# Performance work log

Measured on AMD Instinct MI355X. Metric: run time of the kernel, lower is better.

The kernel has to match this reference:

```python
import jax, jax.numpy as jnp
import numpy as np

# dims: B=batch, S=seq len, H=heads, D=in_features per head, R=realizations, K=conv kernel
B, S, H, D, R, K = 2, 1024, 8, 64, 32, 128


def setup_inputs() -> dict:
    key = jax.random.key(0)
    kq, kk, kwq, kwk, kz = jax.random.split(key, 5)
    queries = jax.random.normal(kq, (B, S, H, D), jnp.float32)
    keys = jax.random.normal(kk, (B, S, H, D), jnp.float32)
    # depthwise conv weights, torch init: uniform[0,1), shape (C_out, 1, K) with groups=C_out
    wq = jax.random.uniform(kwq, (H * D, 1, K), jnp.float32)
    wk = jax.random.uniform(kwk, (H * D, 1, K), jnp.float32)
    # stochastic process noise z: (B*R, H*D, 4K+S), scaled by 1/sqrt(R*D)
    z = jax.random.normal(kz, (B * R, H * D, 4 * K + S), jnp.float32) / np.float32(np.sqrt(R * D))
    return {"queries": queries, "keys": keys, "wq": wq, "wk": wk, "z": z}


def _dwconv(x, w):
    # depthwise 1D cross-correlation, VALID padding (matches nn.Conv1d, groups=C)
    return jax.lax.conv_general_dilated(
        x, w, window_strides=(1,), padding='VALID',
        dimension_numbers=('NCH', 'OIH', 'NCH'),
        feature_group_count=w.shape[0])


def reference(queries, keys, wq, wk, z):
    # note the faithful swap from the source: kbar uses conv_q, qbar uses conv_k
    kbar = _dwconv(z, wq)[:, :, K:K + S].reshape(B, R, H, D, S)
    qbar = _dwconv(z, wk)[:, :, K:K + S].reshape(B, R, H, D, S)
    # fused broadcast-multiply + feature-dim reduction:
    # (qbar * queries[:,None]).sum(axis=3) then permute -> (B,S,H,R)
    qhat = jnp.einsum('brhds,bshd->bshr', qbar, queries)
    khat = jnp.einsum('brhds,bshd->bshr', kbar, keys)
    return qhat, khat
```

## Files before the change

kernel.cpp:

```cpp
#include <hip/hip_runtime.h>

#define BB 2
#define SS 1024
#define HH 8
#define DD 64
#define RR 32
#define KK 128
#define ZLEN 1536
#define HD 512

#define MS 256
#define DC 16
#define NTC 24
#define WROWS 192
#define WSEG (WROWS*DC)
#define PARTS_FLOATS (256*8*2*64*16)

typedef _Float16 f16x8 __attribute__((ext_vector_type(8)));
typedef _Float16 f16x2 __attribute__((ext_vector_type(2)));
typedef float    f32x16 __attribute__((ext_vector_type(16)));

__device__ __forceinline__ void dma16h(const _Float16* g, _Float16* l) {
    const int lane = threadIdx.x & 63;
    __builtin_amdgcn_global_load_lds(
        (const __attribute__((address_space(1))) void*)(g + lane * 8),
        (__attribute__((address_space(3))) void*)l, 16, 0, 0);
}

__global__ __launch_bounds__(256) void wprep_kernel(
    const float* __restrict__ wq, const float* __restrict__ wk,
    _Float16* __restrict__ wqG, _Float16* __restrict__ wkG)
{
    const int tid = threadIdx.x;
    const int h = blockIdx.x & 7, dc = blockIdx.x >> 3;
    #pragma unroll
    for (int i = 0; i < 12; ++i) {
        const int idx = i * 256 + tid;
        const int ti = idx >> 4, di = idx & 15;
        const int tau = ti - 32;
        float vq = 0.f, vk = 0.f;
        if (tau >= 0 && tau < KK) {
            const int src = (h * 64 + dc * 16 + di) * KK + tau;
            vq = wq[src]; vk = wk[src];
        }
        const int dst = (h * 4 + dc) * WSEG + idx;
        wqG[dst] = (_Float16)vq; wkG[dst] = (_Float16)vk;
    }
}

__global__ __launch_bounds__(512) void convspe_mfma(
    const float* __restrict__ q, const float* __restrict__ kmat,
    const _Float16* __restrict__ wqG, const _Float16* __restrict__ wkG,
    const float* __restrict__ z, float* __restrict__ parts)
{
    __shared__ __align__(16) _Float16 zbuf[2][16 * 32 * 16];
    __shared__ __align__(16) _Float16 wqs[WSEG];
    __shared__ __align__(16) _Float16 wks[WSEG];

    const int tid  = threadIdx.x;
    const int wave = tid >> 6;
    const int lane = tid & 63;
    const int rl   = lane & 31;
    const int hi   = lane >> 5;

    const int bx = blockIdx.x;
    const int dc = bx & 3, stile = (bx >> 2) & 3, h = (bx >> 4) & 7, b = bx >> 7;
    const int s0b = stile * MS;
    const int d0  = dc * DC;

    if (wave == 0) {
        const _Float16* seg = wqG + (h * 4 + dc) * WSEG;
        #pragma unroll
        for (int i = 0; i < 6; ++i) dma16h(seg + i * 512, wqs + i * 512);
    } else if (wave == 1) {
        const _Float16* seg = wkG + (h * 4 + dc) * WSEG;
        #pragma unroll
        for (int i = 0; i < 6; ++i) dma16h(seg + i * 512, wks + i * 512);
    }

    f16x8 qf, kf;
    {
        const int s = s0b + wave * 32 + rl;
        const size_t base = (((size_t)b * SS + s) * HH + h) * DD + d0 + 8 * hi;
        #pragma unroll
        for (int j = 0; j < 8; ++j) {
            qf[j] = (_Float16)q[base + j];
            kf[j] = (_Float16)kmat[base + j];
        }
    }

    const int sr  = tid >> 4;
    const int sth = (tid >> 3) & 1;
    const int sdp = tid & 7;
    const float* zr0 = z + ((size_t)(b * RR + sr) * HD + h * DD + d0 + 2 * sdp) * ZLEN
                         + KK + s0b + sth * 8;
    const float* zr1 = zr0 + ZLEN;

    float4 ra[2], rb[2];
    auto loadchunk = [&](int tc) {
        const float4* p0 = (const float4*)(zr0 + tc * 16);
        const float4* p1 = (const float4*)(zr1 + tc * 16);
        #pragma unroll
        for (int i = 0; i < 2; ++i) { ra[i] = p0[i]; rb[i] = p1[i]; }
    };
    auto writechunk = [&](int p) {
        f16x2* dst = (f16x2*)zbuf[p];
        #pragma unroll
        for (int i = 0; i < 2; ++i) {
            const float av[4] = {ra[i].x, ra[i].y, ra[i].z, ra[i].w};
            const float bv[4] = {rb[i].x, rb[i].y, rb[i].z, rb[i].w};
            #pragma unroll
            for (int e = 0; e < 4; ++e) {
                const int ts = sth * 8 + i * 4 + e;
                dst[(ts * 32 + sr) * 8 + sdp] =
                    __builtin_bit_cast(f16x2, __builtin_amdgcn_cvt_pkrtz(av[e], bv[e]));
            }
        }
    };

    f32x16 accq, acck;
    #pragma unroll
    for (int j = 0; j < 16; ++j) { accq[j] = 0.f; acck[j] = 0.f; }

    loadchunk(0);
    writechunk(0);
    loadchunk(1);
    __syncthreads();

    for (int tc = 0; tc < NTC; ++tc) {
        const int p = tc & 1;
        const int tqbase = tc * 16 - wave * 32;
        #pragma unroll 1
        for (int ts = 0; ts < 16; ++ts) {
            const int tau_s = tqbase + ts;
            if (tau_s < 0 || tau_s >= 160) continue;
            const f16x8 a = *(const f16x8*)&zbuf[p][(ts * 32 + rl) * 16 + 8 * hi];
            const int row = tau_s - rl + 32;
            const f16x8 wkf = *(const f16x8*)&wks[row * 16 + 8 * hi];
            const f16x8 wqf = *(const f16x8*)&wqs[row * 16 + 8 * hi];
            accq = __builtin_amdgcn_mfma_f32_32x32x16_f16(a, wkf * qf, accq, 0, 0, 0);
            acck = __builtin_amdgcn_mfma_f32_32x32x16_f16(a, wqf * kf, acck, 0, 0, 0);
        }
        if (tc + 1 < NTC) writechunk((tc + 1) & 1);
        if (tc + 2 < NTC) loadchunk(tc + 2);
        __syncthreads();
    }

    {
        float* pq = parts + ((((size_t)bx * 8 + wave) * 2 + 0) * 64 + lane) * 16;
        float* pk = parts + ((((size_t)bx * 8 + wave) * 2 + 1) * 64 + lane) * 16;
        #pragma unroll
        for (int g = 0; g < 4; ++g) {
            *(float4*)&pq[g * 4] = make_float4(accq[4*g], accq[4*g+1], accq[4*g+2], accq[4*g+3]);
            *(float4*)&pk[g * 4] = make_float4(acck[4*g], acck[4*g+1], acck[4*g+2], acck[4*g+3]);
        }
    }
}

__global__ __launch_bounds__(256) void reduce_kernel(
    const float* __restrict__ parts, float* __restrict__ out)
{
    const int idx = blockIdx.x * 256 + threadIdx.x;
    const int rq = idx & 7, h = (idx >> 3) & 7, s = (idx >> 6) & 1023;
    const int b = (idx >> 16) & 1, o = idx >> 17;
    const int stile = s >> 8, sub = (s >> 5) & 7, rl = s & 31;

    float acc4[4] = {0.f, 0.f, 0.f, 0.f};
    #pragma unroll
    for (int dc = 0; dc < 4; ++dc) {
        const int bx = ((b * 8 + h) * 4 + stile) * 4 + dc;
        const float* pb = parts + (((size_t)bx * 8 + sub) * 2 + o) * 1024;
        #pragma unroll
        for (int i = 0; i < 4; ++i) {
            const int r = rq * 4 + i;
            const int hi2 = (r >> 2) & 1;
            const int reg = (r & 3) + 4 * (r >> 3);
            acc4[i] += pb[(hi2 * 32 + rl) * 16 + reg];
        }
    }
    *(float4*)&out[(size_t)idx * 4] = make_float4(acc4[0], acc4[1], acc4[2], acc4[3]);
}

extern "C" void kernel_launch(void* const* d_in, const int* in_sizes, int n_in,
                              void* d_out, int out_size, void* d_ws, size_t ws_size,
                              hipStream_t stream) {
    const float* q  = (const float*)d_in[0];
    const float* k  = (const float*)d_in[1];
    const float* wq = (const float*)d_in[2];
    const float* wk = (const float*)d_in[3];
    const float* z  = (const float*)d_in[4];
    float* out = (float*)d_out;

    float* parts   = (float*)d_ws;
    _Float16* wqG  = (_Float16*)((char*)d_ws + (size_t)PARTS_FLOATS * 4);
    _Float16* wkG  = wqG + 8 * 4 * WSEG;

    hipLaunchKernelGGL(wprep_kernel, dim3(32), dim3(256), 0, stream, wq, wk, wqG, wkG);
    hipLaunchKernelGGL(convspe_mfma, dim3(256), dim3(512), 0, stream,
                       q, k, wqG, wkG, z, parts);
    hipLaunchKernelGGL(reduce_kernel, dim3(1024), dim3(256), 0, stream, parts, out);
}
```

Measured before the change: 322.6 us.

## Fuse weight prep into conv kernel, software-pipeline MFMA loop, vectorize reduce

Removes the separate weight-prep kernel and has each conv block convert and stage its own fp16 weight slice, with zero padding, directly into LDS. The first z chunk load is issued before the q/k loads so those latencies overlap. The inner MFMA loop drops the per-iteration bounds test by computing the valid range up front and double-buffers its LDS reads in registers. The reduce kernel now reads each partial with one float4 instead of four scalar loads. The cost is redundant weight conversion across the blocks that share a head and d-chunk, plus higher register pressure from the prefetched operands.

```diff
diff --git a/kernel.cpp b/kernel.cpp
--- a/kernel.cpp
+++ b/kernel.cpp
@@ -20,37 +20,9 @@
 typedef _Float16 f16x2 __attribute__((ext_vector_type(2)));
 typedef float    f32x16 __attribute__((ext_vector_type(16)));
 
-__device__ __forceinline__ void dma16h(const _Float16* g, _Float16* l) {
-    const int lane = threadIdx.x & 63;
-    __builtin_amdgcn_global_load_lds(
-        (const __attribute__((address_space(1))) void*)(g + lane * 8),
-        (__attribute__((address_space(3))) void*)l, 16, 0, 0);
-}
-
-__global__ __launch_bounds__(256) void wprep_kernel(
-    const float* __restrict__ wq, const float* __restrict__ wk,
-    _Float16* __restrict__ wqG, _Float16* __restrict__ wkG)
-{
-    const int tid = threadIdx.x;
-    const int h = blockIdx.x & 7, dc = blockIdx.x >> 3;
-    #pragma unroll
-    for (int i = 0; i < 12; ++i) {
-        const int idx = i * 256 + tid;
-        const int ti = idx >> 4, di = idx & 15;
-        const int tau = ti - 32;
-        float vq = 0.f, vk = 0.f;
-        if (tau >= 0 && tau < KK) {
-            const int src = (h * 64 + dc * 16 + di) * KK + tau;
-            vq = wq[src]; vk = wk[src];
-        }
-        const int dst = (h * 4 + dc) * WSEG + idx;
-        wqG[dst] = (_Float16)vq; wkG[dst] = (_Float16)vk;
-    }
-}
-
 __global__ __launch_bounds__(512) void convspe_mfma(
     const float* __restrict__ q, const float* __restrict__ kmat,
-    const _Float16* __restrict__ wqG, const _Float16* __restrict__ wkG,
+    const float* __restrict__ wq, const float* __restrict__ wk,
     const float* __restrict__ z, float* __restrict__ parts)
 {
     __shared__ __align__(16) _Float16 zbuf[2][16 * 32 * 16];
@@ -58,7 +30,7 @@
     __shared__ __align__(16) _Float16 wks[WSEG];
 
     const int tid  = threadIdx.x;
-    const int wave = tid >> 6;
+    const int wave = __builtin_amdgcn_readfirstlane(tid >> 6);
     const int lane = tid & 63;
     const int rl   = lane & 31;
     const int hi   = lane >> 5;
@@ -67,27 +39,6 @@
     const int dc = bx & 3, stile = (bx >> 2) & 3, h = (bx >> 4) & 7, b = bx >> 7;
     const int s0b = stile * MS;
     const int d0  = dc * DC;
-
-    if (wave == 0) {
-        const _Float16* seg = wqG + (h * 4 + dc) * WSEG;
-        #pragma unroll
-        for (int i = 0; i < 6; ++i) dma16h(seg + i * 512, wqs + i * 512);
-    } else if (wave == 1) {
-        const _Float16* seg = wkG + (h * 4 + dc) * WSEG;
-        #pragma unroll
-        for (int i = 0; i < 6; ++i) dma16h(seg + i * 512, wks + i * 512);
-    }
-
-    f16x8 qf, kf;
-    {
-        const int s = s0b + wave * 32 + rl;
-        const size_t base = (((size_t)b * SS + s) * HH + h) * DD + d0 + 8 * hi;
-        #pragma unroll
-        for (int j = 0; j < 8; ++j) {
-            qf[j] = (_Float16)q[base + j];
-            kf[j] = (_Float16)kmat[base + j];
-        }
-    }
 
     const int sr  = tid >> 4;
     const int sth = (tid >> 3) & 1;
@@ -118,11 +69,40 @@
         }
     };
 
+    loadchunk(0);
+
+    f16x8 qf, kf;
+    {
+        const int s = s0b + wave * 32 + rl;
+        const size_t base = (((size_t)b * SS + s) * HH + h) * DD + d0 + 8 * hi;
+        #pragma unroll
+        for (int j = 0; j < 8; ++j) {
+            qf[j] = (_Float16)q[base + j];
+            kf[j] = (_Float16)kmat[base + j];
+        }
+    }
+
+    {
+        const int di = tid & 15, tq = tid >> 4;
+        const int grow = (h * DD + dc * DC + di) * KK + tq * 4;
+        const float4 vq4 = *(const float4*)&wq[grow];
+        const float4 vk4 = *(const float4*)&wk[grow];
+        const float aq[4] = {vq4.x, vq4.y, vq4.z, vq4.w};
+        const float ak[4] = {vk4.x, vk4.y, vk4.z, vk4.w};
+        #pragma unroll
+        for (int e = 0; e < 4; ++e) {
+            const int ds = (tq * 4 + e + 32) * 16 + di;
+            wqs[ds] = (_Float16)aq[e];
+            wks[ds] = (_Float16)ak[e];
+        }
+        wqs[tid] = (_Float16)0.f;        wks[tid] = (_Float16)0.f;
+        wqs[2560 + tid] = (_Float16)0.f; wks[2560 + tid] = (_Float16)0.f;
+    }
+
     f32x16 accq, acck;
     #pragma unroll
     for (int j = 0; j < 16; ++j) { accq[j] = 0.f; acck[j] = 0.f; }
 
-    loadchunk(0);
     writechunk(0);
     loadchunk(1);
     __syncthreads();
@@ -130,16 +110,33 @@
     for (int tc = 0; tc < NTC; ++tc) {
         const int p = tc & 1;
         const int tqbase = tc * 16 - wave * 32;
-        #pragma unroll 1
-        for (int ts = 0; ts < 16; ++ts) {
-            const int tau_s = tqbase + ts;
-            if (tau_s < 0 || tau_s >= 160) continue;
-            const f16x8 a = *(const f16x8*)&zbuf[p][(ts * 32 + rl) * 16 + 8 * hi];
-            const int row = tau_s - rl + 32;
-            const f16x8 wkf = *(const f16x8*)&wks[row * 16 + 8 * hi];
-            const f16x8 wqf = *(const f16x8*)&wqs[row * 16 + 8 * hi];
-            accq = __builtin_amdgcn_mfma_f32_32x32x16_f16(a, wkf * qf, accq, 0, 0, 0);
-            acck = __builtin_amdgcn_mfma_f32_32x32x16_f16(a, wqf * kf, acck, 0, 0, 0);
+        const int lo  = (tqbase < 0) ? -tqbase : 0;
+        const int hi_ = (160 - tqbase < 16) ? (160 - tqbase) : 16;
+        if (lo < hi_) {
+            const _Float16* zb = zbuf[p];
+            auto zrd = [&](int ts) {
+                return *(const f16x8*)&zb[(ts * 32 + rl) * 16 + 8 * hi];
+            };
+            auto wrd = [&](const _Float16* ws, int ts) {
+                const int row = tqbase + ts - rl + 32;
+                return *(const f16x8*)&ws[row * 16 + 8 * hi];
+            };
+            f16x8 a0 = zrd(lo), k0 = wrd(wks, lo), q0 = wrd(wqs, lo);
+            f16x8 a1 = a0, k1 = k0, q1 = q0;
+            if (lo + 1 < hi_) { a1 = zrd(lo + 1); k1 = wrd(wks, lo + 1); q1 = wrd(wqs, lo + 1); }
+            for (int ts = lo; ts < hi_ - 2; ++ts) {
+                const f16x8 a2 = zrd(ts + 2), k2 = wrd(wks, ts + 2), q2 = wrd(wqs, ts + 2);
+                accq = __builtin_amdgcn_mfma_f32_32x32x16_f16(a0, k0 * qf, accq, 0, 0, 0);
+                acck = __builtin_amdgcn_mfma_f32_32x32x16_f16(a0, q0 * kf, acck, 0, 0, 0);
+                a0 = a1; k0 = k1; q0 = q1;
+                a1 = a2; k1 = k2; q1 = q2;
+            }
+            accq = __builtin_amdgcn_mfma_f32_32x32x16_f16(a0, k0 * qf, accq, 0, 0, 0);
+            acck = __builtin_amdgcn_mfma_f32_32x32x16_f16(a0, q0 * kf, acck, 0, 0, 0);
+            if (lo + 1 < hi_) {
+                accq = __builtin_amdgcn_mfma_f32_32x32x16_f16(a1, k1 * qf, accq, 0, 0, 0);
+                acck = __builtin_amdgcn_mfma_f32_32x32x16_f16(a1, q1 * kf, acck, 0, 0, 0);
+            }
         }
         if (tc + 1 < NTC) writechunk((tc + 1) & 1);
         if (tc + 2 < NTC) loadchunk(tc + 2);
@@ -165,20 +162,16 @@
     const int b = (idx >> 16) & 1, o = idx >> 17;
     const int stile = s >> 8, sub = (s >> 5) & 7, rl = s & 31;
 
-    float acc4[4] = {0.f, 0.f, 0.f, 0.f};
+    const int off = ((rq & 1) * 32 + rl) * 16 + 4 * (rq >> 1);
+
+    float4 acc = make_float4(0.f, 0.f, 0.f, 0.f);
     #pragma unroll
     for (int dc = 0; dc < 4; ++dc) {
         const int bx = ((b * 8 + h) * 4 + stile) * 4 + dc;
-        const float* pb = parts + (((size_t)bx * 8 + sub) * 2 + o) * 1024;
-        #pragma unroll
-        for (int i = 0; i < 4; ++i) {
-            const int r = rq * 4 + i;
-            const int hi2 = (r >> 2) & 1;
-            const int reg = (r & 3) + 4 * (r >> 3);
-            acc4[i] += pb[(hi2 * 32 + rl) * 16 + reg];
-        }
+        const float4 v = *(const float4*)&parts[(((size_t)bx * 8 + sub) * 2 + o) * 1024 + off];
+        acc.x += v.x; acc.y += v.y; acc.z += v.z; acc.w += v.w;
     }
-    *(float4*)&out[(size_t)idx * 4] = make_float4(acc4[0], acc4[1], acc4[2], acc4[3]);
+    *(float4*)&out[(size_t)idx * 4] = acc;
 }
 
 extern "C" void kernel_launch(void* const* d_in, const int* in_sizes, int n_in,
@@ -191,12 +184,9 @@
     const float* z  = (const float*)d_in[4];
     float* out = (float*)d_out;
 
-    float* parts   = (float*)d_ws;
-    _Float16* wqG  = (_Float16*)((char*)d_ws + (size_t)PARTS_FLOATS * 4);
-    _Float16* wkG  = wqG + 8 * 4 * WSEG;
+    float* parts = (float*)d_ws;
 
-    hipLaunchKernelGGL(wprep_kernel, dim3(32), dim3(256), 0, stream, wq, wk, wqG, wkG);
     hipLaunchKernelGGL(convspe_mfma, dim3(256), dim3(512), 0, stream,
-                       q, k, wqG, wkG, z, parts);
+                       q, k, wq, wk, z, parts);
     hipLaunchKernelGGL(reduce_kernel, dim3(1024), dim3(256), 0, stream, parts, out);
 }
```

Measured after the change: 306.6 us. -5.0%, faster.
